# Optimization experiments

Hardware: AMD Instinct MI355X
Metric: run time of the kernel (lower is better)

The kernel has to match this reference:

```python
import jax, jax.numpy as jnp
import numpy as np

D_MODEL = 768
NUM_HEADS = 12
HEAD_DIM = D_MODEL // NUM_HEADS


def setup_inputs() -> dict:
    key = jax.random.key(0)
    ks = jax.random.split(key, 9)
    B, S = 2, 2048
    s = 1.0 / np.sqrt(D_MODEL)
    x = jax.random.normal(ks[0], (B, S, D_MODEL), dtype=jnp.float32)
    Wq = jax.random.normal(ks[1], (D_MODEL, D_MODEL), dtype=jnp.float32) * s
    Wk = jax.random.normal(ks[2], (D_MODEL, D_MODEL), dtype=jnp.float32) * s
    Wv = jax.random.normal(ks[3], (D_MODEL, D_MODEL), dtype=jnp.float32) * s
    Wo = jax.random.normal(ks[4], (D_MODEL, D_MODEL), dtype=jnp.float32) * s
    bq = jax.random.normal(ks[5], (D_MODEL,), dtype=jnp.float32) * 0.01
    bk = jax.random.normal(ks[6], (D_MODEL,), dtype=jnp.float32) * 0.01
    bv = jax.random.normal(ks[7], (D_MODEL,), dtype=jnp.float32) * 0.01
    bo = jax.random.normal(ks[8], (D_MODEL,), dtype=jnp.float32) * 0.01
    return {"x": x, "Wq": Wq, "bq": bq, "Wk": Wk, "bk": bk,
            "Wv": Wv, "bv": bv, "Wo": Wo, "bo": bo}


def reference(x, Wq, bq, Wk, bk, Wv, bv, Wo, bo):
    B, S, _ = x.shape
    # projections; reshape to [B, H, S, Dh]
    def split_heads(t):
        return t.reshape(B, S, NUM_HEADS, HEAD_DIM).transpose(0, 2, 1, 3)
    q = split_heads(x @ Wq + bq)
    k = split_heads(x @ Wk + bk)
    v = split_heads(x @ Wv + bv)
    scale = 1.0 / np.sqrt(HEAD_DIM)
    scores = jnp.einsum("bhqd,bhkd->bhqk", q, k) * scale  # [B,H,S,S]
    attn = jax.nn.softmax(scores, axis=-1)
    # dropout p=0.0 (eval) -> identity
    ctx = jnp.einsum("bhqk,bhkd->bhqd", attn, v)
    ctx = ctx.transpose(0, 2, 1, 3).reshape(B, S, D_MODEL)
    return ctx @ Wo + bo
```

## Files before the change

kernel.cpp:

```cpp
#include <hip/hip_runtime.h>
#include <hip/hip_bf16.h>
#include <hip/hip_fp16.h>

#define D_MODEL 768
#define NHEADS  12
#define HD      64
#define BATCH   2
#define SEQ     2048
#define NTOK    (BATCH*SEQ)
#define NX      ((size_t)NTOK * D_MODEL)
#define NW      ((size_t)D_MODEL * D_MODEL)
#define SC_LOG2 0.18033688f

typedef __attribute__((ext_vector_type(8))) short    short8;
typedef __attribute__((ext_vector_type(8))) _Float16 half8;
typedef __attribute__((ext_vector_type(2))) __fp16   fp16x2;
typedef __attribute__((ext_vector_type(4))) float    f32x4;

__device__ __forceinline__ float bf2f(short s) {
    union { unsigned u; float f; } c;
    c.u = ((unsigned)(unsigned short)s) << 16;
    return c.f;
}
__device__ __forceinline__ short f2bf(float f) {
    __hip_bfloat16 h = __float2bfloat16(f);
    return *(short*)&h;
}

#ifdef __has_builtin
#if __has_builtin(__builtin_amdgcn_global_load_lds)
#define HAS_GLD 1
#endif
#if __has_builtin(__builtin_amdgcn_exp2f)
#define EXP2(x) __builtin_amdgcn_exp2f(x)
#else
#define EXP2(x) exp2f(x)
#endif
#if __has_builtin(__builtin_amdgcn_cvt_pkrtz)
#define HAS_PKRTZ 1
#endif
#else
#define EXP2(x) exp2f(x)
#endif
#ifdef HAS_GLD
#define GLD16(gp, lp) __builtin_amdgcn_global_load_lds( \
    (const __attribute__((address_space(1))) void*)(gp), \
    (__attribute__((address_space(3))) void*)(lp), 16, 0, 0)
#endif

__global__ __launch_bounds__(256) void fused_conv(
        const void* __restrict__ xin,
        const void* __restrict__ w0, const void* __restrict__ w1,
        const void* __restrict__ w2, const void* __restrict__ w3,
        const void* __restrict__ b0, const void* __restrict__ b1,
        const void* __restrict__ b2, const void* __restrict__ b3,
        short* __restrict__ xc, short* __restrict__ wt,
        short* __restrict__ bc, int* __restrict__ flag)
{
    __shared__ int red[256];
    __shared__ float T[64][65];
    const int tid = threadIdx.x;
    const int F = blockIdx.x;

    {
        const short* xs = (const short*)xin;
        int maxe = 0;
#pragma unroll
        for (int u = 0; u < 16; ++u) {
            int e = ((unsigned short)xs[tid * 16 + u] >> 7) & 0xFF;
            maxe = max(maxe, e);
        }
        red[tid] = maxe;
        __syncthreads();
        for (int s = 128; s > 0; s >>= 1) {
            if (tid < s) red[tid] = max(red[tid], red[tid + s]);
            __syncthreads();
        }
    }
    const bool isf = (red[0] > 140);

    if (F < 3072) {
        const int i = F * 256 + tid;
        if (isf) {
            float4 f = ((const float4*)xin)[i];
            short4 o = { f2bf(f.x), f2bf(f.y), f2bf(f.z), f2bf(f.w) };
            ((short4*)xc)[i] = o;
        } else {
            ((short4*)xc)[i] = ((const short4*)xin)[i];
        }
    } else if (F < 3648) {
        const int G = F - 3072;
        const int z = G / 144, rr = G % 144;
        const int k0 = (rr % 12) * 64, n0 = (rr / 12) * 64;
        const void* src = (z == 0) ? w0 : (z == 1) ? w1 : (z == 2) ? w2 : w3;
        const float sc = (z == 0) ? SC_LOG2 : 1.0f;
        const int la = tid & 15, lb = tid >> 4;
#pragma unroll
        for (int u = 0; u < 4; ++u) {
            const int kr = (lb & 3) + 4 * u + 16 * (lb >> 2);
            if (isf) {
                float4 f = *(const float4*)((const float*)src + (size_t)(k0 + kr) * D_MODEL + n0 + la * 4);
                T[kr][la*4+0] = f.x; T[kr][la*4+1] = f.y; T[kr][la*4+2] = f.z; T[kr][la*4+3] = f.w;
            } else {
                short4 s = *(const short4*)((const short*)src + (size_t)(k0 + kr) * D_MODEL + n0 + la * 4);
                T[kr][la*4+0] = bf2f(s.x); T[kr][la*4+1] = bf2f(s.y);
                T[kr][la*4+2] = bf2f(s.z); T[kr][la*4+3] = bf2f(s.w);
            }
        }
        __syncthreads();
#pragma unroll
        for (int u = 0; u < 4; ++u) {
            const int nr = (lb & 3) + 4 * u + 16 * (lb >> 2);
            short4 o = { f2bf(T[la*4+0][nr] * sc), f2bf(T[la*4+1][nr] * sc),
                         f2bf(T[la*4+2][nr] * sc), f2bf(T[la*4+3][nr] * sc) };
            *(short4*)(wt + (size_t)z * NW + (size_t)(n0 + nr) * D_MODEL + k0 + la * 4) = o;
        }
    } else {
        if (tid == 0) *flag = isf ? 1 : 0;
        const void* srcs[4] = { b0, b1, b2, b3 };
        for (int z = 0; z < 4; ++z) {
            const float sc = (z == 0) ? SC_LOG2 : 1.0f;
            for (int i = tid; i < D_MODEL; i += 256) {
                float v = isf ? ((const float*)srcs[z])[i] : bf2f(((const short*)srcs[z])[i]);
                bc[z * D_MODEL + i] = f2bf(v * sc);
            }
        }
    }
}

__global__ __launch_bounds__(256) void qkv_gemm(const short* __restrict__ X,
                                                const short* __restrict__ Wt,
                                                const short* __restrict__ bias,
                                                short* __restrict__ qb,
                                                short* __restrict__ kb,
                                                _Float16* __restrict__ Vt)
{
    __shared__ __align__(16) char shbuf[24576];
    short* Als = (short*)shbuf;
    short* Bls = (short*)(shbuf + 8192);
    _Float16* T = (_Float16*)shbuf;

    const int tid = threadIdx.x;
    const int wave = tid >> 6, lane = tid & 63;
    const int quad = lane >> 4, l16 = lane & 15;
    const int wm = wave & 1, wn = wave >> 1;
    const int m0 = blockIdx.x * 64;
    const int ng = blockIdx.y * 128;

    f32x4 acc[2][4];
#pragma unroll
    for (int nt = 0; nt < 4; ++nt) {
        const float bv = bf2f(bias[ng + wn*64 + nt*16 + l16]);
#pragma unroll
        for (int mt = 0; mt < 2; ++mt) acc[mt][nt] = (f32x4){bv, bv, bv, bv};
    }

    const int row = tid >> 2, ch = (tid & 3) * 8;
#ifdef HAS_GLD
#define QSTAGE(buf, k0) do { \
        GLD16(X  + (size_t)(m0 + row)      * D_MODEL + (k0) + ch, &Als[(buf)*2048 + tid*8]); \
        GLD16(Wt + (size_t)(ng + row)      * D_MODEL + (k0) + ch, &Bls[(buf)*4096 + tid*8]); \
        GLD16(Wt + (size_t)(ng + 64 + row) * D_MODEL + (k0) + ch, &Bls[(buf)*4096 + 2048 + tid*8]); \
    } while (0)
#else
#define QSTAGE(buf, k0) do { \
        short8 r0 = *(const short8*)(X  + (size_t)(m0 + row)      * D_MODEL + (k0) + ch); \
        short8 r2 = *(const short8*)(Wt + (size_t)(ng + row)      * D_MODEL + (k0) + ch); \
        short8 r3 = *(const short8*)(Wt + (size_t)(ng + 64 + row) * D_MODEL + (k0) + ch); \
        *(short8*)&Als[(buf)*2048 + tid*8] = r0; \
        *(short8*)&Bls[(buf)*4096 + tid*8] = r2; \
        *(short8*)&Bls[(buf)*4096 + 2048 + tid*8] = r3; \
    } while (0)
#endif

    QSTAGE(0, 0);
    __syncthreads();

    for (int ks = 0; ks < 24; ++ks) {
        const int cur = ks & 1;
        if (ks + 1 < 24) QSTAGE(cur ^ 1, (ks + 1) * 32);

        short8 a[2], b[4];
#pragma unroll
        for (int mt = 0; mt < 2; ++mt)
            a[mt] = *(const short8*)&Als[cur*2048 + (wm*32 + mt*16 + l16) * 32 + quad*8];
#pragma unroll
        for (int nt = 0; nt < 4; ++nt)
            b[nt] = *(const short8*)&Bls[cur*4096 + (wn*64 + nt*16 + l16) * 32 + quad*8];
#pragma unroll
        for (int mt = 0; mt < 2; ++mt)
#pragma unroll
        for (int nt = 0; nt < 4; ++nt)
            acc[mt][nt] = __builtin_amdgcn_mfma_f32_16x16x32_bf16(a[mt], b[nt], acc[mt][nt], 0, 0, 0);

        __syncthreads();
    }
#undef QSTAGE

    const int seg = blockIdx.y / 6;
    if (seg < 2) {
        short* out = seg ? kb : qb;
        const int nl = ng - seg * 768;
#pragma unroll
        for (int mt = 0; mt < 2; ++mt)
#pragma unroll
        for (int nt = 0; nt < 4; ++nt) {
            const int n = nl + wn*64 + nt*16 + l16;
#pragma unroll
            for (int r = 0; r < 4; ++r) {
                const int m = m0 + wm*32 + mt*16 + quad*4 + r;
                out[(size_t)m * D_MODEL + n] = f2bf(acc[mt][nt][r]);
            }
        }
    } else {
        const int batch = m0 >> 11, tokb = m0 & (SEQ - 1);
#pragma unroll
        for (int nt = 0; nt < 4; ++nt) {
            const int dim_l = wn*64 + nt*16 + l16;
#pragma unroll
            for (int mt = 0; mt < 2; ++mt) {
                const int tok_l = wm*32 + mt*16 + quad*4;
                union { _Float16 h4[4]; int2 v; } u;
#pragma unroll
                for (int r = 0; r < 4; ++r) u.h4[r] = (_Float16)acc[mt][nt][r];
                *(int2*)&T[dim_l * 72 + tok_l] = u.v;
            }
        }
        __syncthreads();
#pragma unroll
        for (int u = 0; u < 4; ++u) {
            const int slot = tid + u * 256;
            const int drow = slot >> 3, chk = slot & 7;
            int4 val = *(const int4*)&T[drow * 72 + chk * 8];
            const int dim_g = ng - 1536 + drow;
            const int h = dim_g >> 6, d = dim_g & 63;
            *(int4*)(Vt + ((size_t)(batch * NHEADS + h) * HD + d) * SEQ + tokb + chk*8) = val;
        }
    }
}

__global__ __launch_bounds__(256) void out_gemm(const short* __restrict__ X,
                                                const short* __restrict__ Wt,
                                                const short* __restrict__ bias,
                                                void* __restrict__ outv,
                                                const int* __restrict__ flag)
{
    __shared__ short Als[2][2048];
    __shared__ short Bls[2][2048];

    const int tid = threadIdx.x;
    const int wave = tid >> 6, lane = tid & 63;
    const int quad = lane >> 4, l16 = lane & 15;
    const int m0 = blockIdx.x * 64;
    const int n0 = blockIdx.y * 64;

    f32x4 acc[4];
#pragma unroll
    for (int nt = 0; nt < 4; ++nt) {
        const float bv = bf2f(bias[n0 + nt*16 + l16]);
        acc[nt] = (f32x4){bv, bv, bv, bv};
    }

    const int row = tid >> 2, ch = (tid & 3) * 8;
#ifdef HAS_GLD
#define OSTAGE(buf, k0) do { \
        GLD16(X  + (size_t)(m0 + row) * D_MODEL + (k0) + ch, &Als[buf][tid*8]); \
        GLD16(Wt + (size_t)(n0 + row) * D_MODEL + (k0) + ch, &Bls[buf][tid*8]); \
    } while (0)
#else
#define OSTAGE(buf, k0) do { \
        short8 r0 = *(const short8*)(X  + (size_t)(m0 + row) * D_MODEL + (k0) + ch); \
        short8 r1 = *(const short8*)(Wt + (size_t)(n0 + row) * D_MODEL + (k0) + ch); \
        *(short8*)&Als[buf][tid*8] = r0; \
        *(short8*)&Bls[buf][tid*8] = r1; \
    } while (0)
#endif

    OSTAGE(0, 0);
    __syncthreads();

    for (int ks = 0; ks < 24; ++ks) {
        const int cur = ks & 1;
        if (ks + 1 < 24) OSTAGE(cur ^ 1, (ks + 1) * 32);

        short8 a = *(const short8*)&Als[cur][(wave*16 + l16) * 32 + quad*8];
#pragma unroll
        for (int nt = 0; nt < 4; ++nt) {
            short8 b = *(const short8*)&Bls[cur][(nt*16 + l16) * 32 + quad*8];
            acc[nt] = __builtin_amdgcn_mfma_f32_16x16x32_bf16(a, b, acc[nt], 0, 0, 0);
        }
        __syncthreads();
    }
#undef OSTAGE

    const bool outf32 = (*flag != 0);
#pragma unroll
    for (int nt = 0; nt < 4; ++nt) {
        const int n = n0 + nt*16 + l16;
#pragma unroll
        for (int r = 0; r < 4; ++r) {
            const int m = m0 + wave*16 + quad*4 + r;
            const size_t idx = (size_t)m * D_MODEL + n;
            if (outf32) ((float*)outv)[idx] = acc[nt][r];
            else        ((short*)outv)[idx] = f2bf(acc[nt][r]);
        }
    }
}

__global__ __launch_bounds__(256) void attn_mfma(const short* __restrict__ q,
                                                 const short* __restrict__ k,
                                                 const _Float16* __restrict__ Vt,
                                                 short* __restrict__ ctx)
{
    __shared__ short    Kls[2][64 * 64];
    __shared__ _Float16 Vls[2][64 * 64];
    __shared__ _Float16 Pls[4][16 * 64];

    const int tid  = threadIdx.x;
    const int wave = tid >> 6, lane = tid & 63;
    const int quad = lane >> 4, l16 = lane & 15;

    const int F = blockIdx.x;
    const int xcd = F & 7, slot = F >> 3;
    const int bh = xcd * 3 + (slot >> 5);
    const int q0 = (slot & 31) * 64;
    const int b = bh / NHEADS, h = bh % NHEADS;
    const size_t bS = (size_t)b * SEQ;
    const int myq = q0 + wave * 16 + l16;

    short8 qf[2];
#pragma unroll
    for (int k0h = 0; k0h < 2; ++k0h)
        qf[k0h] = *(const short8*)(q + (bS + myq) * D_MODEL + h*HD + k0h*32 + quad*8);

    half8 ones;
#pragma unroll
    for (int j = 0; j < 8; ++j) ones[j] = (_Float16)1.0f;

    const int s0 = tid, s1 = tid + 256;
    const int kr0 = s0 >> 3, kc0 = (s0 & 7) ^ (kr0 & 7);
    const int kr1 = s1 >> 3, kc1 = (s1 & 7) ^ (kr1 & 7);
    const short*    kg0 = k  + (bS + kr0) * D_MODEL + h*HD + kc0*8;
    const short*    kg1 = k  + (bS + kr1) * D_MODEL + h*HD + kc1*8;
    const _Float16* vg0 = Vt + ((size_t)bh * HD + kr0) * SEQ + kc0*8;
    const _Float16* vg1 = Vt + ((size_t)bh * HD + kr1) * SEQ + kc1*8;

#ifdef HAS_GLD
#define STAGE(buf, j0) do { \
        GLD16(kg0 + (size_t)(j0) * D_MODEL, &Kls[buf][s0 * 8]); \
        GLD16(kg1 + (size_t)(j0) * D_MODEL, &Kls[buf][s1 * 8]); \
        GLD16(vg0 + (j0),                   &Vls[buf][s0 * 8]); \
        GLD16(vg1 + (j0),                   &Vls[buf][s1 * 8]); \
    } while (0)
#else
#define STAGE(buf, j0) do { \
        short8 a_ = *(const short8*)(kg0 + (size_t)(j0) * D_MODEL); \
        short8 b_ = *(const short8*)(kg1 + (size_t)(j0) * D_MODEL); \
        half8  c_ = *(const half8*)(vg0 + (j0)); \
        half8  d_ = *(const half8*)(vg1 + (j0)); \
        *(short8*)&Kls[buf][s0 * 8] = a_;  *(short8*)&Kls[buf][s1 * 8] = b_; \
        *(half8*)&Vls[buf][s0 * 8] = c_;   *(half8*)&Vls[buf][s1 * 8] = d_; \
    } while (0)
#endif

    float m_ = -1e30f;
    f32x4 lacc = (f32x4){0.f, 0.f, 0.f, 0.f};
    f32x4 o[4];
#pragma unroll
    for (int t = 0; t < 4; ++t) o[t] = (f32x4){0.f, 0.f, 0.f, 0.f};

    STAGE(0, 0);
    __syncthreads();

    for (int jt = 0; jt < SEQ / 64; ++jt) {
        const int cur = jt & 1;
        if (jt + 1 < SEQ / 64) STAGE(cur ^ 1, (jt + 1) * 64);

        f32x4 s4[4];
#pragma unroll
        for (int t = 0; t < 4; ++t) s4[t] = (f32x4){0.f, 0.f, 0.f, 0.f};
#pragma unroll
        for (int k0h = 0; k0h < 2; ++k0h)
#pragma unroll
        for (int t = 0; t < 4; ++t) {
            const int krow = t*16 + l16;
            short8 kf = *(const short8*)&Kls[cur][krow*64 + (((k0h*4 + quad) ^ (krow & 7)) * 8)];
            s4[t] = __builtin_amdgcn_mfma_f32_16x16x32_bf16(kf, qf[k0h], s4[t], 0, 0, 0);
        }

        float mx = s4[0][0];
#pragma unroll
        for (int t = 0; t < 4; ++t)
#pragma unroll
        for (int r = 0; r < 4; ++r) mx = fmaxf(mx, s4[t][r]);
        if (__any(mx > m_)) {
#pragma unroll
            for (int d = 1; d < 64; d <<= 1) mx = fmaxf(mx, __shfl_xor(mx, d));
            const float mn = fmaxf(m_, mx);
            const float al = EXP2(m_ - mn);
#pragma unroll
            for (int t = 0; t < 4; ++t) {
                o[t][0] *= al; o[t][1] *= al; o[t][2] *= al; o[t][3] *= al;
            }
            lacc[0] *= al; lacc[1] *= al; lacc[2] *= al; lacc[3] *= al;
            m_ = mn;
        }

#pragma unroll
        for (int t = 0; t < 4; ++t) {
            union { fp16x2 h2[2]; int2 v; } u4;
#ifdef HAS_PKRTZ
            u4.h2[0] = __builtin_amdgcn_cvt_pkrtz(EXP2(s4[t][0] - m_), EXP2(s4[t][1] - m_));
            u4.h2[1] = __builtin_amdgcn_cvt_pkrtz(EXP2(s4[t][2] - m_), EXP2(s4[t][3] - m_));
#else
            u4.h2[0] = (fp16x2){ (__fp16)EXP2(s4[t][0] - m_), (__fp16)EXP2(s4[t][1] - m_) };
            u4.h2[1] = (fp16x2){ (__fp16)EXP2(s4[t][2] - m_), (__fp16)EXP2(s4[t][3] - m_) };
#endif
            const int c = (t*2 + (quad >> 1)) ^ (l16 & 7);
            *(int2*)&Pls[wave][l16*64 + c*8 + (quad & 1)*4] = u4.v;
        }

#pragma unroll
        for (int k0h = 0; k0h < 2; ++k0h) {
            const int pc = (k0h*4 + quad) ^ (l16 & 7);
            half8 pf = *(half8*)&Pls[wave][l16*64 + pc*8];
            lacc = __builtin_amdgcn_mfma_f32_16x16x32_f16(ones, pf, lacc, 0, 0, 0);
#pragma unroll
            for (int t = 0; t < 4; ++t) {
                const int vrow = t*16 + l16;
                half8 vf = *(const half8*)&Vls[cur][vrow*64 + (((k0h*4 + quad) ^ (vrow & 7)) * 8)];
                o[t] = __builtin_amdgcn_mfma_f32_16x16x32_f16(vf, pf, o[t], 0, 0, 0);
            }
        }

        __syncthreads();
    }

    const float inv = 1.0f / lacc[0];
    const size_t rowp = (bS + myq) * D_MODEL + h*HD;
#pragma unroll
    for (int t = 0; t < 4; ++t) {
        union { short s4v[4]; int2 v; } u4;
#pragma unroll
        for (int r = 0; r < 4; ++r) u4.s4v[r] = f2bf(o[t][r] * inv);
        *(int2*)(ctx + rowp + t*16 + quad*4) = u4.v;
    }
#undef STAGE
}

extern "C" void kernel_launch(void* const* d_in, const int* in_sizes, int n_in,
                              void* d_out, int out_size, void* d_ws, size_t ws_size,
                              hipStream_t stream)
{
    int* flag = (int*)d_ws;
    short* xc = (short*)((char*)d_ws + 64);
    short* Wt = xc + NX;
    short* bc = Wt + 4 * NW;
    short* qb = bc + 4 * D_MODEL;
    short* kb = qb + NX;
    _Float16* Vt = (_Float16*)(kb + NX);
    short* cb = (short*)(Vt + NX);

    fused_conv<<<3649, 256, 0, stream>>>(d_in[0],
                                         d_in[1], d_in[3], d_in[5], d_in[7],
                                         d_in[2], d_in[4], d_in[6], d_in[8],
                                         xc, Wt, bc, flag);

    qkv_gemm<<<dim3(NTOK/64, 2304/128), 256, 0, stream>>>(xc, Wt, bc, qb, kb, Vt);

    attn_mfma<<<768, 256, 0, stream>>>(qb, kb, Vt, cb);

    out_gemm<<<dim3(NTOK/64, D_MODEL/64), 256, 0, stream>>>(cb, Wt + 3*NW, bc + 3*D_MODEL, d_out, flag);
}
```

Measured before the change: 178.1 us.

## Software-pipeline QK^T one tile ahead with triple-buffered V in attention

Restructures the attention loop so the QK^T MFMAs for tile j+1 are issued before the softmax and PV work of tile j. K stays double-buffered while V becomes triple-buffered, which lets loads run two tiles ahead. The aim is to overlap matrix-core work with the exp and max math and with global-to-LDS loads. It also adds a lazy rescale threshold (only rescale when the row max grows by more than 8 in log2 units) and a launch-bounds occupancy hint of 3. The costs are higher register pressure from two score buffers, extra LDS, and a risk of fp16 overflow in P because of the lazy threshold.

After: 174.1 us. -2.3%, faster.

```diff
diff --git a/kernel.cpp b/kernel.cpp
--- a/kernel.cpp
+++ b/kernel.cpp
@@ -46,6 +46,12 @@
 #define GLD16(gp, lp) __builtin_amdgcn_global_load_lds( \
     (const __attribute__((address_space(1))) void*)(gp), \
     (__attribute__((address_space(3))) void*)(lp), 16, 0, 0)
+#endif
+
+#ifdef HAS_PKRTZ
+#define PKF16(a, b) __builtin_amdgcn_cvt_pkrtz((a), (b))
+#else
+#define PKF16(a, b) ((fp16x2){ (__fp16)(a), (__fp16)(b) })
 #endif
 
 __global__ __launch_bounds__(256) void fused_conv(
@@ -307,13 +313,13 @@
     }
 }
 
-__global__ __launch_bounds__(256) void attn_mfma(const short* __restrict__ q,
-                                                 const short* __restrict__ k,
-                                                 const _Float16* __restrict__ Vt,
-                                                 short* __restrict__ ctx)
+__global__ __launch_bounds__(256, 3) void attn_mfma(const short* __restrict__ q,
+                                                    const short* __restrict__ k,
+                                                    const _Float16* __restrict__ Vt,
+                                                    short* __restrict__ ctx)
 {
     __shared__ short    Kls[2][64 * 64];
-    __shared__ _Float16 Vls[2][64 * 64];
+    __shared__ _Float16 Vls[3][64 * 64];
     __shared__ _Float16 Pls[4][16 * 64];
 
     const int tid  = threadIdx.x;
@@ -346,19 +352,23 @@
     const _Float16* vg1 = Vt + ((size_t)bh * HD + kr1) * SEQ + kc1*8;
 
 #ifdef HAS_GLD
-#define STAGE(buf, j0) do { \
+#define STAGE_K(buf, j0) do { \
         GLD16(kg0 + (size_t)(j0) * D_MODEL, &Kls[buf][s0 * 8]); \
         GLD16(kg1 + (size_t)(j0) * D_MODEL, &Kls[buf][s1 * 8]); \
-        GLD16(vg0 + (j0),                   &Vls[buf][s0 * 8]); \
-        GLD16(vg1 + (j0),                   &Vls[buf][s1 * 8]); \
-    } while (0)
-#else
-#define STAGE(buf, j0) do { \
+    } while (0)
+#define STAGE_V(buf, j0) do { \
+        GLD16(vg0 + (j0), &Vls[buf][s0 * 8]); \
+        GLD16(vg1 + (j0), &Vls[buf][s1 * 8]); \
+    } while (0)
+#else
+#define STAGE_K(buf, j0) do { \
         short8 a_ = *(const short8*)(kg0 + (size_t)(j0) * D_MODEL); \
         short8 b_ = *(const short8*)(kg1 + (size_t)(j0) * D_MODEL); \
+        *(short8*)&Kls[buf][s0 * 8] = a_;  *(short8*)&Kls[buf][s1 * 8] = b_; \
+    } while (0)
+#define STAGE_V(buf, j0) do { \
         half8  c_ = *(const half8*)(vg0 + (j0)); \
         half8  d_ = *(const half8*)(vg1 + (j0)); \
-        *(short8*)&Kls[buf][s0 * 8] = a_;  *(short8*)&Kls[buf][s1 * 8] = b_; \
         *(half8*)&Vls[buf][s0 * 8] = c_;   *(half8*)&Vls[buf][s1 * 8] = d_; \
     } while (0)
 #endif
@@ -369,71 +379,82 @@
 #pragma unroll
     for (int t = 0; t < 4; ++t) o[t] = (f32x4){0.f, 0.f, 0.f, 0.f};
 
-    STAGE(0, 0);
+    f32x4 sA[4], sB[4];
+
+#define QK(S, KB) do { \
+    _Pragma("unroll") \
+    for (int t = 0; t < 4; ++t) S[t] = (f32x4){0.f, 0.f, 0.f, 0.f}; \
+    _Pragma("unroll") \
+    for (int k0h = 0; k0h < 2; ++k0h) \
+    _Pragma("unroll") \
+    for (int t = 0; t < 4; ++t) { \
+        const int krow = t*16 + l16; \
+        short8 kf = *(const short8*)&Kls[KB][krow*64 + (((k0h*4 + quad) ^ (krow & 7)) * 8)]; \
+        S[t] = __builtin_amdgcn_mfma_f32_16x16x32_bf16(kf, qf[k0h], S[t], 0, 0, 0); \
+    } \
+} while (0)
+
+#define BODY(JT, SCUR, SNXT) do { \
+    if ((JT) + 2 < SEQ/64) { \
+        STAGE_K(((JT) + 2) & 1, ((JT) + 2) * 64); \
+        STAGE_V(((JT) + 2) % 3, ((JT) + 2) * 64); \
+    } \
+    if ((JT) + 1 < SEQ/64) QK(SNXT, ((JT) + 1) & 1); \
+    { \
+         \
+        float mx = SCUR[0][0]; \
+        _Pragma("unroll") \
+        for (int t = 0; t < 4; ++t) \
+        _Pragma("unroll") \
+        for (int r = 0; r < 4; ++r) mx = fmaxf(mx, SCUR[t][r]); \
+        if (__any(mx > m_ + 8.f)) { \
+            _Pragma("unroll") \
+            for (int d = 1; d < 64; d <<= 1) mx = fmaxf(mx, __shfl_xor(mx, d)); \
+            const float mn = fmaxf(m_, mx); \
+            const float al = EXP2(m_ - mn); \
+            _Pragma("unroll") \
+            for (int t = 0; t < 4; ++t) { \
+                o[t][0] *= al; o[t][1] *= al; o[t][2] *= al; o[t][3] *= al; \
+            } \
+            lacc[0] *= al; lacc[1] *= al; lacc[2] *= al; lacc[3] *= al; \
+            m_ = mn; \
+        } \
+         \
+        _Pragma("unroll") \
+        for (int t = 0; t < 4; ++t) { \
+            union { fp16x2 h2[2]; int2 v; } u4; \
+            u4.h2[0] = PKF16(EXP2(SCUR[t][0] - m_), EXP2(SCUR[t][1] - m_)); \
+            u4.h2[1] = PKF16(EXP2(SCUR[t][2] - m_), EXP2(SCUR[t][3] - m_)); \
+            const int c = (t*2 + (quad >> 1)) ^ (l16 & 7); \
+            *(int2*)&Pls[wave][l16*64 + c*8 + (quad & 1)*4] = u4.v; \
+        } \
+         \
+        const int vb = (JT) % 3; \
+        _Pragma("unroll") \
+        for (int k0h = 0; k0h < 2; ++k0h) { \
+            const int pc = (k0h*4 + quad) ^ (l16 & 7); \
+            half8 pf = *(half8*)&Pls[wave][l16*64 + pc*8]; \
+            lacc = __builtin_amdgcn_mfma_f32_16x16x32_f16(ones, pf, lacc, 0, 0, 0); \
+            _Pragma("unroll") \
+            for (int t = 0; t < 4; ++t) { \
+                const int vrow = t*16 + l16; \
+                half8 vf = *(const half8*)&Vls[vb][vrow*64 + (((k0h*4 + quad) ^ (vrow & 7)) * 8)]; \
+                o[t] = __builtin_amdgcn_mfma_f32_16x16x32_f16(vf, pf, o[t], 0, 0, 0); \
+            } \
+        } \
+    } \
+    __syncthreads(); \
+} while (0)
+
+    STAGE_K(0, 0); STAGE_V(0, 0);
     __syncthreads();
-
-    for (int jt = 0; jt < SEQ / 64; ++jt) {
-        const int cur = jt & 1;
-        if (jt + 1 < SEQ / 64) STAGE(cur ^ 1, (jt + 1) * 64);
-
-        f32x4 s4[4];
-#pragma unroll
-        for (int t = 0; t < 4; ++t) s4[t] = (f32x4){0.f, 0.f, 0.f, 0.f};
-#pragma unroll
-        for (int k0h = 0; k0h < 2; ++k0h)
-#pragma unroll
-        for (int t = 0; t < 4; ++t) {
-            const int krow = t*16 + l16;
-            short8 kf = *(const short8*)&Kls[cur][krow*64 + (((k0h*4 + quad) ^ (krow & 7)) * 8)];
-            s4[t] = __builtin_amdgcn_mfma_f32_16x16x32_bf16(kf, qf[k0h], s4[t], 0, 0, 0);
-        }
-
-        float mx = s4[0][0];
-#pragma unroll
-        for (int t = 0; t < 4; ++t)
-#pragma unroll
-        for (int r = 0; r < 4; ++r) mx = fmaxf(mx, s4[t][r]);
-        if (__any(mx > m_)) {
-#pragma unroll
-            for (int d = 1; d < 64; d <<= 1) mx = fmaxf(mx, __shfl_xor(mx, d));
-            const float mn = fmaxf(m_, mx);
-            const float al = EXP2(m_ - mn);
-#pragma unroll
-            for (int t = 0; t < 4; ++t) {
-                o[t][0] *= al; o[t][1] *= al; o[t][2] *= al; o[t][3] *= al;
-            }
-            lacc[0] *= al; lacc[1] *= al; lacc[2] *= al; lacc[3] *= al;
-            m_ = mn;
-        }
-
-#pragma unroll
-        for (int t = 0; t < 4; ++t) {
-            union { fp16x2 h2[2]; int2 v; } u4;
-#ifdef HAS_PKRTZ
-            u4.h2[0] = __builtin_amdgcn_cvt_pkrtz(EXP2(s4[t][0] - m_), EXP2(s4[t][1] - m_));
-            u4.h2[1] = __builtin_amdgcn_cvt_pkrtz(EXP2(s4[t][2] - m_), EXP2(s4[t][3] - m_));
-#else
-            u4.h2[0] = (fp16x2){ (__fp16)EXP2(s4[t][0] - m_), (__fp16)EXP2(s4[t][1] - m_) };
-            u4.h2[1] = (fp16x2){ (__fp16)EXP2(s4[t][2] - m_), (__fp16)EXP2(s4[t][3] - m_) };
-#endif
-            const int c = (t*2 + (quad >> 1)) ^ (l16 & 7);
-            *(int2*)&Pls[wave][l16*64 + c*8 + (quad & 1)*4] = u4.v;
-        }
-
-#pragma unroll
-        for (int k0h = 0; k0h < 2; ++k0h) {
-            const int pc = (k0h*4 + quad) ^ (l16 & 7);
-            half8 pf = *(half8*)&Pls[wave][l16*64 + pc*8];
-            lacc = __builtin_amdgcn_mfma_f32_16x16x32_f16(ones, pf, lacc, 0, 0, 0);
-#pragma unroll
-            for (int t = 0; t < 4; ++t) {
-                const int vrow = t*16 + l16;
-                half8 vf = *(const half8*)&Vls[cur][vrow*64 + (((k0h*4 + quad) ^ (vrow & 7)) * 8)];
-                o[t] = __builtin_amdgcn_mfma_f32_16x16x32_f16(vf, pf, o[t], 0, 0, 0);
-            }
-        }
-
-        __syncthreads();
+    STAGE_K(1, 64); STAGE_V(1, 64);
+    QK(sA, 0);
+    __syncthreads();
+
+    for (int jt = 0; jt < SEQ / 64; jt += 2) {
+        BODY(jt,     sA, sB);
+        BODY(jt + 1, sB, sA);
     }
 
     const float inv = 1.0f / lacc[0];
@@ -445,7 +466,10 @@
         for (int r = 0; r < 4; ++r) u4.s4v[r] = f2bf(o[t][r] * inv);
         *(int2*)(ctx + rowp + t*16 + quad*4) = u4.v;
     }
-#undef STAGE
+#undef BODY
+#undef QK
+#undef STAGE_K
+#undef STAGE_V
 }
 
 extern "C" void kernel_launch(void* const* d_in, const int* in_sizes, int n_in,
```
